# Optimization experiments

Measured on AMD Instinct MI355X. Metric: run time of the kernel, lower is better.

Reference implementation:

```python
import jax, jax.numpy as jnp
import numpy as np

N_EMBD = 1024
NUM_HEADS = 16
HEAD_SIZE = 64
B, T, T_ENC = 2, 2048, 2048


def setup_inputs() -> dict:
    key = jax.random.key(0)
    k1, k2, k3, k4, k5 = jax.random.split(key, 5)
    scale = 1.0 / np.sqrt(N_EMBD)
    return {
        "x_enc": jax.random.normal(k1, (B, T_ENC, N_EMBD), dtype=jnp.float32),
        "x": jax.random.normal(k2, (B, T, N_EMBD), dtype=jnp.float32),
        "Wk": jax.random.normal(k3, (N_EMBD, NUM_HEADS * HEAD_SIZE), dtype=jnp.float32) * scale,
        "Wq": jax.random.normal(k4, (N_EMBD, NUM_HEADS * HEAD_SIZE), dtype=jnp.float32) * scale,
        "Wv": jax.random.normal(k5, (N_EMBD, NUM_HEADS * HEAD_SIZE), dtype=jnp.float32) * scale,
    }


def reference(x_enc, x, Wk, Wq, Wv):
    b, t, c = x.shape
    _, t_enc, _ = x_enc.shape
    # projections (bias-free linears)
    k = (x_enc @ Wk).reshape(b, t_enc, NUM_HEADS, HEAD_SIZE)  # [B,S,H,D]
    v = (x_enc @ Wv).reshape(b, t_enc, NUM_HEADS, HEAD_SIZE)
    q = (x @ Wq).reshape(b, t, NUM_HEADS, HEAD_SIZE)          # [B,T,H,D]
    # NOTE: original scales by C**-0.5 with C = n_embd (not head_size)
    scale = jnp.asarray(c, x.dtype) ** -0.5
    wei = jnp.einsum("bthd,bshd->bhts", q, k) * scale          # [B,H,T,S]
    wei = jax.nn.softmax(wei, axis=-1)
    out = jnp.einsum("bhts,bshd->bthd", wei, v)                # [B,T,H,D]
    return out
```

## Files before the change

### kernel.cpp

```cpp
#include <hip/hip_runtime.h>
#include <hip/hip_bf16.h>
#include <stdint.h>

#define NE 1024
#define NH 16
#define HD 64
#define BB 2
#define TT 2048
#define MM (BB*TT)

typedef __attribute__((ext_vector_type(8))) short short8;
typedef __attribute__((ext_vector_type(4))) float floatx4;

__device__ __forceinline__ short f2bf(float f) {
    union { float f; uint32_t u; } v; v.f = f;
    uint32_t u = v.u;
    return (short)((u + 0x7fffu + ((u >> 16) & 1u)) >> 16);
}

__device__ __forceinline__ float fast_exp2(float x) {
#if __has_builtin(__builtin_amdgcn_exp2f)
    return __builtin_amdgcn_exp2f(x);
#else
    float r; asm("v_exp_f32 %0, %1" : "=v"(r) : "v"(x)); return r;
#endif
}

__device__ __forceinline__ void gload_lds16(const void* g, void* l) {
    __builtin_amdgcn_global_load_lds((__attribute__((address_space(1))) void*)g,
                                     (__attribute__((address_space(3))) void*)l,
                                     16, 0, 0);
}

__global__ void cvt_bf16(const float* __restrict__ in, short* __restrict__ out, int n8) {
    int i = blockIdx.x * blockDim.x + threadIdx.x;
    if (i >= n8) return;
    const floatx4* p = (const floatx4*)(in + (size_t)i * 8);
    floatx4 a = p[0], b = p[1];
    union { uint32_t u[4]; short8 s; } r;
    asm("v_cvt_pk_bf16_f32 %0, %1, %2" : "=v"(r.u[0]) : "v"(a[0]), "v"(a[1]));
    asm("v_cvt_pk_bf16_f32 %0, %1, %2" : "=v"(r.u[1]) : "v"(a[2]), "v"(a[3]));
    asm("v_cvt_pk_bf16_f32 %0, %1, %2" : "=v"(r.u[2]) : "v"(b[0]), "v"(b[1]));
    asm("v_cvt_pk_bf16_f32 %0, %1, %2" : "=v"(r.u[3]) : "v"(b[2]), "v"(b[3]));
    *(short8*)(out + (size_t)i * 8) = r.s;
}

__global__ void wtrans(const float* __restrict__ Wq, const float* __restrict__ Wk,
                       const float* __restrict__ Wv, short* __restrict__ Wt) {
    __shared__ float t[32][33];
    const float* W = blockIdx.z == 0 ? Wq : (blockIdx.z == 1 ? Wk : Wv);
    short* dst = Wt + (size_t)blockIdx.z * NE * NE;
    int n0 = blockIdx.x * 32, k0 = blockIdx.y * 32;
    int tx = threadIdx.x & 31, ty = threadIdx.x >> 5;
    #pragma unroll
    for (int i = 0; i < 4; i++)
        t[ty * 4 + i][tx] = W[(size_t)(k0 + ty * 4 + i) * NE + n0 + tx];
    __syncthreads();
    #pragma unroll
    for (int i = 0; i < 4; i++)
        dst[(size_t)(n0 + ty * 4 + i) * NE + k0 + tx] = f2bf(t[tx][ty * 4 + i]);
}

__global__ void __launch_bounds__(256) gemm_bt(const short* __restrict__ x_bf,
                                               const short* __restrict__ xenc_bf,
                                               const short* __restrict__ Wt,
                                               short* __restrict__ qkv) {
    __shared__ short sA[128 * 32];
    __shared__ short sB[128 * 32];
    const int z = blockIdx.z;
    const short* A  = (z == 0) ? x_bf : xenc_bf;
    const short* Bt = Wt + (size_t)z * NE * NE;
    short* C = qkv + (size_t)z * MM * NE;
    const float osc = (z == 0) ? 0.04508422f : 1.0f;

    const int tid = threadIdx.x;
    const int lane = tid & 63, wid = tid >> 6;
    const int l15 = lane & 15, lg = lane >> 4;
    const int wr = wid >> 1, wc = wid & 1;
    const int m0 = blockIdx.y * 128, n0 = blockIdx.x * 128;

    const short* gA = A  + (size_t)(m0 + (tid >> 2)) * NE + (tid & 3) * 8;
    const short* gB = Bt + (size_t)(n0 + (tid >> 2)) * NE + (tid & 3) * 8;
    short* lA = sA + wid * 512;
    short* lB = sB + wid * 512;

    floatx4 acc[4][4];
    floatx4 zero = {0.f, 0.f, 0.f, 0.f};
    #pragma unroll
    for (int i = 0; i < 4; i++)
        #pragma unroll
        for (int j = 0; j < 4; j++) acc[i][j] = zero;

    for (int kt = 0; kt < NE; kt += 32) {
        gload_lds16(gA + kt,            lA);
        gload_lds16(gA + 64 * NE + kt,  lA + 2048);
        gload_lds16(gB + kt,            lB);
        gload_lds16(gB + 64 * NE + kt,  lB + 2048);
        __syncthreads();
        short8 af[4], bfr[4];
        #pragma unroll
        for (int i = 0; i < 4; i++) {
            af[i]  = *(const short8*)&sA[(wr * 64 + i * 16 + l15) * 32 + lg * 8];
            bfr[i] = *(const short8*)&sB[(wc * 64 + i * 16 + l15) * 32 + lg * 8];
        }
        #pragma unroll
        for (int i = 0; i < 4; i++)
            #pragma unroll
            for (int j = 0; j < 4; j++)
                acc[i][j] = __builtin_amdgcn_mfma_f32_16x16x32_bf16(af[i], bfr[j], acc[i][j], 0, 0, 0);
        __syncthreads();
    }
    #pragma unroll
    for (int i = 0; i < 4; i++)
        #pragma unroll
        for (int j = 0; j < 4; j++)
            #pragma unroll
            for (int r = 0; r < 4; r++) {
                int row = m0 + wr * 64 + i * 16 + lg * 4 + r;
                int col = n0 + wc * 64 + j * 16 + l15;
                C[(size_t)row * NE + col] = f2bf(acc[i][j][r] * osc);
            }
}

__global__ void vtrans(const short* __restrict__ v, short* __restrict__ vt) {
    __shared__ short t[64][65];
    int s0 = blockIdx.x * 64;
    int bh = blockIdx.y;
    int b = bh >> 4, h = bh & 15;
    int tid = threadIdx.x;
    int c = tid & 63, rr = tid >> 6;
    #pragma unroll
    for (int i = 0; i < 16; i++)
        t[i * 4 + rr][c] = v[(size_t)(b * TT + s0 + i * 4 + rr) * NE + h * HD + c];
    __syncthreads();
    int csw = (c & 35) | (((c >> 4) & 1) << 2) | (((c >> 2) & 3) << 3);
    #pragma unroll
    for (int i = 0; i < 16; i++)
        vt[(size_t)(bh * HD + i * 4 + rr) * TT + s0 + csw] = t[c][i * 4 + rr];
}

__global__ void __launch_bounds__(256, 2) fattn(const short* __restrict__ q,
                                                const short* __restrict__ k,
                                                const short* __restrict__ vt,
                                                float* __restrict__ out) {
    __shared__ short kbuf[3][4096];
    __shared__ short vbuf[3][4096];
    const int tid = threadIdx.x, lane = tid & 63, wid = tid >> 6;
    const int l15 = lane & 15, lg = lane >> 4;
    const int q0 = blockIdx.x * 128 + wid * 32;
    const int bh = blockIdx.y, b = bh >> 4, h = bh & 15;

    short8 qf[2][2];
    #pragma unroll
    for (int qb = 0; qb < 2; qb++) {
        const short* qp = q + (size_t)(b * TT + q0 + qb * 16 + l15) * NE + h * HD + lg * 8;
        qf[qb][0] = *(const short8*)qp;
        qf[qb][1] = *(const short8*)(qp + 32);
    }
    short8 ones;
    #pragma unroll
    for (int j = 0; j < 8; j++) ones[j] = (short)0x3F80;

    floatx4 acc_o[2][4];
    floatx4 acc_l[2];
    floatx4 zero = {0.f, 0.f, 0.f, 0.f};
    floatx4 minus8 = {-8.f, -8.f, -8.f, -8.f};
    #pragma unroll
    for (int qb = 0; qb < 2; qb++) {
        acc_l[qb] = zero;
        #pragma unroll
        for (int db = 0; db < 4; db++) acc_o[qb][db] = zero;
    }

    const char* kgb = (const char*)(k + (size_t)(b * TT) * NE + h * HD);
    const char* vgb = (const char*)(vt + (size_t)bh * HD * TT);
    const int srow = tid >> 3;
    const int ssw  = ((tid & 7) * 16) ^ ((srow & 7) << 4);
    const char* ksrc = kgb + (size_t)srow * (NE * 2) + ssw;
    const char* vsrc = vgb + (size_t)srow * (TT * 2) + ssw;

    const int swz  = (l15 & 7) << 4;
    const int rd0  = l15 * 128 + ((lg * 16) ^ swz);
    const int rd1  = l15 * 128 + ((64 + lg * 16) ^ swz);

#define STAGE(bi, s0v) do { \
    const char* ks_ = ksrc + (size_t)(s0v) * (NE * 2); \
    gload_lds16(ks_,                 &kbuf[bi][wid * 512]); \
    gload_lds16(ks_ + 32 * (NE * 2), &kbuf[bi][wid * 512 + 2048]); \
    const char* vs_ = vsrc + (size_t)(s0v) * 2; \
    gload_lds16(vs_,                 &vbuf[bi][wid * 512]); \
    gload_lds16(vs_ + 32 * (TT * 2), &vbuf[bi][wid * 512 + 2048]); \
} while (0)

#define FATTN_COMPUTE(cur) do { \
    const char* kb = (const char*)kbuf[cur]; \
    const char* vb = (const char*)vbuf[cur]; \
    short8 kf[4][2]; \
    _Pragma("unroll") \
    for (int cb = 0; cb < 4; cb++) { \
        kf[cb][0] = *(const short8*)(kb + cb * 2048 + rd0); \
        kf[cb][1] = *(const short8*)(kb + cb * 2048 + rd1); \
    } \
    floatx4 sacc[2][4]; \
    _Pragma("unroll") \
    for (int qb = 0; qb < 2; qb++) \
        _Pragma("unroll") \
        for (int cb = 0; cb < 4; cb++) sacc[qb][cb] = minus8; \
    __builtin_amdgcn_s_setprio(1); \
    _Pragma("unroll") \
    for (int qb = 0; qb < 2; qb++) \
        _Pragma("unroll") \
        for (int cb = 0; cb < 4; cb++) { \
            sacc[qb][cb] = __builtin_amdgcn_mfma_f32_16x16x32_bf16(kf[cb][0], qf[qb][0], sacc[qb][cb], 0, 0, 0); \
            sacc[qb][cb] = __builtin_amdgcn_mfma_f32_16x16x32_bf16(kf[cb][1], qf[qb][1], sacc[qb][cb], 0, 0, 0); \
        } \
    __builtin_amdgcn_s_setprio(0); \
    short8 vf[2][4]; \
    _Pragma("unroll") \
    for (int db = 0; db < 4; db++) { \
        vf[0][db] = *(const short8*)(vb + db * 2048 + rd0); \
        vf[1][db] = *(const short8*)(vb + db * 2048 + rd1); \
    } \
    short8 paf[2][2]; \
    _Pragma("unroll") \
    for (int qb = 0; qb < 2; qb++) { \
        float pe[16]; \
        _Pragma("unroll") \
        for (int cb = 0; cb < 4; cb++) \
            _Pragma("unroll") \
            for (int r = 0; r < 4; r++) \
                pe[cb * 4 + r] = fast_exp2(sacc[qb][cb][r]); \
        _Pragma("unroll") \
        for (int ks = 0; ks < 2; ks++) { \
            union { uint32_t u[4]; short8 s; } pk_; \
            _Pragma("unroll") \
            for (int j2 = 0; j2 < 4; j2++) \
                asm("v_cvt_pk_bf16_f32 %0, %1, %2" \
                    : "=v"(pk_.u[j2]) \
                    : "v"(pe[ks * 8 + 2 * j2]), "v"(pe[ks * 8 + 2 * j2 + 1])); \
            paf[qb][ks] = pk_.s; \
        } \
    } \
    __builtin_amdgcn_s_setprio(1); \
    _Pragma("unroll") \
    for (int qb = 0; qb < 2; qb++) \
        _Pragma("unroll") \
        for (int ks = 0; ks < 2; ks++) { \
            _Pragma("unroll") \
            for (int db = 0; db < 4; db++) \
                acc_o[qb][db] = __builtin_amdgcn_mfma_f32_16x16x32_bf16(paf[qb][ks], vf[ks][db], acc_o[qb][db], 0, 0, 0); \
            acc_l[qb] = __builtin_amdgcn_mfma_f32_16x16x32_bf16(paf[qb][ks], ones, acc_l[qb], 0, 0, 0); \
        } \
    __builtin_amdgcn_s_setprio(0); \
} while (0)

    STAGE(0, 0);
    STAGE(1, 64);
    for (int t = 0; t < 31; ++t) {
        asm volatile("s_waitcnt vmcnt(4)" ::: "memory");
        __builtin_amdgcn_sched_barrier(0);
        __builtin_amdgcn_s_barrier();
        __builtin_amdgcn_sched_barrier(0);
        if (t < 30) STAGE((t + 2) % 3, (t + 2) * 64);
        FATTN_COMPUTE(t % 3);
    }
    asm volatile("s_waitcnt vmcnt(0)" ::: "memory");
    __builtin_amdgcn_sched_barrier(0);
    __builtin_amdgcn_s_barrier();
    __builtin_amdgcn_sched_barrier(0);
    FATTN_COMPUTE(1);
#undef STAGE
#undef FATTN_COMPUTE

    #pragma unroll
    for (int qb = 0; qb < 2; qb++) {
        #pragma unroll
        for (int r = 0; r < 4; r++) {
            float inv = 1.0f / acc_l[qb][r];
            #pragma unroll
            for (int db = 0; db < 4; db++)
                out[(size_t)(b * TT + q0 + qb * 16 + lg * 4 + r) * NE + h * HD + db * 16 + l15] =
                    acc_o[qb][db][r] * inv;
        }
    }
}

extern "C" void kernel_launch(void* const* d_in, const int* in_sizes, int n_in,
                              void* d_out, int out_size, void* d_ws, size_t ws_size,
                              hipStream_t stream) {
    const float* x_enc = (const float*)d_in[0];
    const float* x     = (const float*)d_in[1];
    const float* Wk    = (const float*)d_in[2];
    const float* Wq    = (const float*)d_in[3];
    const float* Wv    = (const float*)d_in[4];
    float* out = (float*)d_out;

    const size_t SZ = (size_t)MM * NE;
    short* x_bf    = (short*)d_ws;
    short* xenc_bf = x_bf + SZ;
    short* Wt      = xenc_bf + SZ;
    short* qkv     = Wt + 3 * (size_t)NE * NE;
    short* vt      = qkv + 3 * SZ;

    cvt_bf16<<<dim3(2048), dim3(256), 0, stream>>>(x,     x_bf,    (int)(SZ / 8));
    cvt_bf16<<<dim3(2048), dim3(256), 0, stream>>>(x_enc, xenc_bf, (int)(SZ / 8));
    wtrans<<<dim3(32, 32, 3), dim3(256), 0, stream>>>(Wq, Wk, Wv, Wt);
    gemm_bt<<<dim3(8, 32, 3), dim3(256), 0, stream>>>(x_bf, xenc_bf, Wt, qkv);
    vtrans<<<dim3(32, 32), dim3(256), 0, stream>>>(qkv + 2 * SZ, vt);
    fattn<<<dim3(16, 32), dim3(256), 0, stream>>>(qkv, qkv + SZ, vt, out);
}
```

Before: 101.6 us.

## Triple-buffer projection GEMM loads and halve queries per attention block

The projection GEMM now uses a three-stage LDS ring with async global-to-LDS loads and a single barrier per k-step, plus raised MFMA priority, replacing the load-sync-compute-sync loop so that loads overlap compute. The attention kernel now gives each wave 16 queries instead of 32 and launches twice as many blocks. This raises parallelism and lowers register pressure, but each block loads K/V for half as many queries, so K/V traffic is doubled.

```diff
diff --git a/kernel.cpp b/kernel.cpp
--- a/kernel.cpp
+++ b/kernel.cpp
@@ -65,8 +65,8 @@
                                                const short* __restrict__ xenc_bf,
                                                const short* __restrict__ Wt,
                                                short* __restrict__ qkv) {
-    __shared__ short sA[128 * 32];
-    __shared__ short sB[128 * 32];
+    __shared__ short sA[3][4096];
+    __shared__ short sB[3][4096];
     const int z = blockIdx.z;
     const short* A  = (z == 0) ? x_bf : xenc_bf;
     const short* Bt = Wt + (size_t)z * NE * NE;
@@ -81,8 +81,6 @@
 
     const short* gA = A  + (size_t)(m0 + (tid >> 2)) * NE + (tid & 3) * 8;
     const short* gB = Bt + (size_t)(n0 + (tid >> 2)) * NE + (tid & 3) * 8;
-    short* lA = sA + wid * 512;
-    short* lB = sB + wid * 512;
 
     floatx4 acc[4][4];
     floatx4 zero = {0.f, 0.f, 0.f, 0.f};
@@ -91,25 +89,47 @@
         #pragma unroll
         for (int j = 0; j < 4; j++) acc[i][j] = zero;
 
-    for (int kt = 0; kt < NE; kt += 32) {
-        gload_lds16(gA + kt,            lA);
-        gload_lds16(gA + 64 * NE + kt,  lA + 2048);
-        gload_lds16(gB + kt,            lB);
-        gload_lds16(gB + 64 * NE + kt,  lB + 2048);
-        __syncthreads();
-        short8 af[4], bfr[4];
-        #pragma unroll
-        for (int i = 0; i < 4; i++) {
-            af[i]  = *(const short8*)&sA[(wr * 64 + i * 16 + l15) * 32 + lg * 8];
-            bfr[i] = *(const short8*)&sB[(wc * 64 + i * 16 + l15) * 32 + lg * 8];
-        }
-        #pragma unroll
-        for (int i = 0; i < 4; i++)
-            #pragma unroll
-            for (int j = 0; j < 4; j++)
-                acc[i][j] = __builtin_amdgcn_mfma_f32_16x16x32_bf16(af[i], bfr[j], acc[i][j], 0, 0, 0);
-        __syncthreads();
+#define GSTAGE(bi, kt) do { \
+    gload_lds16(gA + (kt),            &sA[bi][wid * 512]); \
+    gload_lds16(gA + 64 * NE + (kt),  &sA[bi][wid * 512 + 2048]); \
+    gload_lds16(gB + (kt),            &sB[bi][wid * 512]); \
+    gload_lds16(gB + 64 * NE + (kt),  &sB[bi][wid * 512 + 2048]); \
+} while (0)
+
+#define GCOMP(cur) do { \
+    short8 af[4], bfr[4]; \
+    _Pragma("unroll") \
+    for (int i = 0; i < 4; i++) { \
+        af[i]  = *(const short8*)&sA[cur][(wr * 64 + i * 16 + l15) * 32 + lg * 8]; \
+        bfr[i] = *(const short8*)&sB[cur][(wc * 64 + i * 16 + l15) * 32 + lg * 8]; \
+    } \
+    __builtin_amdgcn_s_setprio(1); \
+    _Pragma("unroll") \
+    for (int i = 0; i < 4; i++) \
+        _Pragma("unroll") \
+        for (int j = 0; j < 4; j++) \
+            acc[i][j] = __builtin_amdgcn_mfma_f32_16x16x32_bf16(af[i], bfr[j], acc[i][j], 0, 0, 0); \
+    __builtin_amdgcn_s_setprio(0); \
+} while (0)
+
+    GSTAGE(0, 0);
+    GSTAGE(1, 32);
+    for (int t = 0; t < 31; ++t) {
+        asm volatile("s_waitcnt vmcnt(4)" ::: "memory");
+        __builtin_amdgcn_sched_barrier(0);
+        __builtin_amdgcn_s_barrier();
+        __builtin_amdgcn_sched_barrier(0);
+        if (t < 30) GSTAGE((t + 2) % 3, (t + 2) * 32);
+        GCOMP(t % 3);
     }
+    asm volatile("s_waitcnt vmcnt(0)" ::: "memory");
+    __builtin_amdgcn_sched_barrier(0);
+    __builtin_amdgcn_s_barrier();
+    __builtin_amdgcn_sched_barrier(0);
+    GCOMP(1);
+#undef GSTAGE
+#undef GCOMP
+
     #pragma unroll
     for (int i = 0; i < 4; i++)
         #pragma unroll
@@ -147,30 +167,24 @@
     __shared__ short vbuf[3][4096];
     const int tid = threadIdx.x, lane = tid & 63, wid = tid >> 6;
     const int l15 = lane & 15, lg = lane >> 4;
-    const int q0 = blockIdx.x * 128 + wid * 32;
+    const int q0 = blockIdx.x * 64 + wid * 16;
     const int bh = blockIdx.y, b = bh >> 4, h = bh & 15;
 
-    short8 qf[2][2];
-    #pragma unroll
-    for (int qb = 0; qb < 2; qb++) {
-        const short* qp = q + (size_t)(b * TT + q0 + qb * 16 + l15) * NE + h * HD + lg * 8;
-        qf[qb][0] = *(const short8*)qp;
-        qf[qb][1] = *(const short8*)(qp + 32);
-    }
+    const short* qp = q + (size_t)(b * TT + q0 + l15) * NE + h * HD + lg * 8;
+    short8 qf0 = *(const short8*)qp;
+    short8 qf1 = *(const short8*)(qp + 32);
+
     short8 ones;
     #pragma unroll
     for (int j = 0; j < 8; j++) ones[j] = (short)0x3F80;
 
-    floatx4 acc_o[2][4];
-    floatx4 acc_l[2];
+    floatx4 acc_o[4];
+    floatx4 acc_l;
     floatx4 zero = {0.f, 0.f, 0.f, 0.f};
     floatx4 minus8 = {-8.f, -8.f, -8.f, -8.f};
-    #pragma unroll
-    for (int qb = 0; qb < 2; qb++) {
-        acc_l[qb] = zero;
-        #pragma unroll
-        for (int db = 0; db < 4; db++) acc_o[qb][db] = zero;
-    }
+    acc_l = zero;
+    #pragma unroll
+    for (int db = 0; db < 4; db++) acc_o[db] = zero;
 
     const char* kgb = (const char*)(k + (size_t)(b * TT) * NE + h * HD);
     const char* vgb = (const char*)(vt + (size_t)bh * HD * TT);
@@ -201,19 +215,15 @@
         kf[cb][0] = *(const short8*)(kb + cb * 2048 + rd0); \
         kf[cb][1] = *(const short8*)(kb + cb * 2048 + rd1); \
     } \
-    floatx4 sacc[2][4]; \
-    _Pragma("unroll") \
-    for (int qb = 0; qb < 2; qb++) \
-        _Pragma("unroll") \
-        for (int cb = 0; cb < 4; cb++) sacc[qb][cb] = minus8; \
+    floatx4 sacc[4]; \
+    _Pragma("unroll") \
+    for (int cb = 0; cb < 4; cb++) sacc[cb] = minus8; \
     __builtin_amdgcn_s_setprio(1); \
     _Pragma("unroll") \
-    for (int qb = 0; qb < 2; qb++) \
-        _Pragma("unroll") \
-        for (int cb = 0; cb < 4; cb++) { \
-            sacc[qb][cb] = __builtin_amdgcn_mfma_f32_16x16x32_bf16(kf[cb][0], qf[qb][0], sacc[qb][cb], 0, 0, 0); \
-            sacc[qb][cb] = __builtin_amdgcn_mfma_f32_16x16x32_bf16(kf[cb][1], qf[qb][1], sacc[qb][cb], 0, 0, 0); \
-        } \
+    for (int cb = 0; cb < 4; cb++) { \
+        sacc[cb] = __builtin_amdgcn_mfma_f32_16x16x32_bf16(kf[cb][0], qf0, sacc[cb], 0, 0, 0); \
+        sacc[cb] = __builtin_amdgcn_mfma_f32_16x16x32_bf16(kf[cb][1], qf1, sacc[cb], 0, 0, 0); \
+    } \
     __builtin_amdgcn_s_setprio(0); \
     short8 vf[2][4]; \
     _Pragma("unroll") \
@@ -221,36 +231,31 @@
         vf[0][db] = *(const short8*)(vb + db * 2048 + rd0); \
         vf[1][db] = *(const short8*)(vb + db * 2048 + rd1); \
     } \
-    short8 paf[2][2]; \
-    _Pragma("unroll") \
-    for (int qb = 0; qb < 2; qb++) { \
-        float pe[16]; \
+    float pe[16]; \
+    _Pragma("unroll") \
+    for (int cb = 0; cb < 4; cb++) \
         _Pragma("unroll") \
-        for (int cb = 0; cb < 4; cb++) \
-            _Pragma("unroll") \
-            for (int r = 0; r < 4; r++) \
-                pe[cb * 4 + r] = fast_exp2(sacc[qb][cb][r]); \
+        for (int r = 0; r < 4; r++) \
+            pe[cb * 4 + r] = fast_exp2(sacc[cb][r]); \
+    short8 paf[2]; \
+    _Pragma("unroll") \
+    for (int ks = 0; ks < 2; ks++) { \
+        union { uint32_t u[4]; short8 s; } pk_; \
         _Pragma("unroll") \
-        for (int ks = 0; ks < 2; ks++) { \
-            union { uint32_t u[4]; short8 s; } pk_; \
-            _Pragma("unroll") \
-            for (int j2 = 0; j2 < 4; j2++) \
-                asm("v_cvt_pk_bf16_f32 %0, %1, %2" \
-                    : "=v"(pk_.u[j2]) \
-                    : "v"(pe[ks * 8 + 2 * j2]), "v"(pe[ks * 8 + 2 * j2 + 1])); \
-            paf[qb][ks] = pk_.s; \
-        } \
+        for (int j2 = 0; j2 < 4; j2++) \
+            asm("v_cvt_pk_bf16_f32 %0, %1, %2" \
+                : "=v"(pk_.u[j2]) \
+                : "v"(pe[ks * 8 + 2 * j2]), "v"(pe[ks * 8 + 2 * j2 + 1])); \
+        paf[ks] = pk_.s; \
     } \
     __builtin_amdgcn_s_setprio(1); \
     _Pragma("unroll") \
-    for (int qb = 0; qb < 2; qb++) \
+    for (int ks = 0; ks < 2; ks++) { \
         _Pragma("unroll") \
-        for (int ks = 0; ks < 2; ks++) { \
-            _Pragma("unroll") \
-            for (int db = 0; db < 4; db++) \
-                acc_o[qb][db] = __builtin_amdgcn_mfma_f32_16x16x32_bf16(paf[qb][ks], vf[ks][db], acc_o[qb][db], 0, 0, 0); \
-            acc_l[qb] = __builtin_amdgcn_mfma_f32_16x16x32_bf16(paf[qb][ks], ones, acc_l[qb], 0, 0, 0); \
-        } \
+        for (int db = 0; db < 4; db++) \
+            acc_o[db] = __builtin_amdgcn_mfma_f32_16x16x32_bf16(paf[ks], vf[ks][db], acc_o[db], 0, 0, 0); \
+        acc_l = __builtin_amdgcn_mfma_f32_16x16x32_bf16(paf[ks], ones, acc_l, 0, 0, 0); \
+    } \
     __builtin_amdgcn_s_setprio(0); \
 } while (0)
 
@@ -273,15 +278,12 @@
 #undef FATTN_COMPUTE
 
     #pragma unroll
-    for (int qb = 0; qb < 2; qb++) {
+    for (int r = 0; r < 4; r++) {
+        float inv = 1.0f / acc_l[r];
         #pragma unroll
-        for (int r = 0; r < 4; r++) {
-            float inv = 1.0f / acc_l[qb][r];
-            #pragma unroll
-            for (int db = 0; db < 4; db++)
-                out[(size_t)(b * TT + q0 + qb * 16 + lg * 4 + r) * NE + h * HD + db * 16 + l15] =
-                    acc_o[qb][db][r] * inv;
-        }
+        for (int db = 0; db < 4; db++)
+            out[(size_t)(b * TT + q0 + lg * 4 + r) * NE + h * HD + db * 16 + l15] =
+                acc_o[db][r] * inv;
     }
 }
 
@@ -307,5 +309,5 @@
     wtrans<<<dim3(32, 32, 3), dim3(256), 0, stream>>>(Wq, Wk, Wv, Wt);
     gemm_bt<<<dim3(8, 32, 3), dim3(256), 0, stream>>>(x_bf, xenc_bf, Wt, qkv);
     vtrans<<<dim3(32, 32), dim3(256), 0, stream>>>(qkv + 2 * SZ, vt);
-    fattn<<<dim3(16, 32), dim3(256), 0, stream>>>(qkv, qkv + SZ, vt, out);
-}
+    fattn<<<dim3(32, 32), dim3(256), 0, stream>>>(qkv, qkv + SZ, vt, out);
+}
```

Measured after the change: 114.1 us. 1.12x slower.
